# Kernel optimization log

Measured on AMD Instinct MI355X. Metric: run time of the kernel, lower is better.

Reference implementation:

```python
import jax, jax.numpy as jnp
import numpy as np

B, T, D, H = 4, 2048, 1024, 16
HD = D // H  # head dim = 64

def setup_inputs() -> dict:
    key = jax.random.key(0)
    ks = jax.random.split(key, 4)
    scale = 1.0 / np.sqrt(D)
    return {
        "hidden_states": jax.random.normal(ks[0], (B, T, D), dtype=jnp.float32),
        "attention_mask": jnp.zeros((B, 1, 1, T), dtype=jnp.float32),
        "Wq": jax.random.normal(ks[1], (D, D), dtype=jnp.float32) * scale,
        "bq": jnp.zeros((D,), dtype=jnp.float32),
        "Wk": jax.random.normal(ks[2], (D, D), dtype=jnp.float32) * scale,
        "bk": jnp.zeros((D,), dtype=jnp.float32),
        "Wv": jax.random.normal(ks[3], (D, D), dtype=jnp.float32) * scale,
        "bv": jnp.zeros((D,), dtype=jnp.float32),
    }

def _split_heads(x):
    # [B, T, D] -> [B, H, T, HD]
    b, t, _ = x.shape
    return x.reshape(b, t, H, HD).transpose(0, 2, 1, 3)

def reference(hidden_states, attention_mask, Wq, bq, Wk, bk, Wv, bv):
    q = _split_heads(hidden_states @ Wq.T + bq)
    k = _split_heads(hidden_states @ Wk.T + bk)
    v = _split_heads(hidden_states @ Wv.T + bv)
    # scores: [B, H, T, T]
    scores = jnp.einsum("bhqd,bhkd->bhqk", q, k) * (HD ** -0.5)
    t = hidden_states.shape[1]
    causal = jnp.triu(jnp.ones((t, t), dtype=bool), k=1)  # True above diagonal -> masked
    scores = jnp.where(causal[None, None], -jnp.inf, scores)
    scores = scores + attention_mask  # additive padding mask [B,1,1,T]
    probs = jax.nn.softmax(scores, axis=-1)
    out = jnp.einsum("bhqk,bhkd->bhqd", probs, v)
    # [B, H, T, HD] -> [B, T, D]
    return out.transpose(0, 2, 1, 3).reshape(hidden_states.shape[0], t, D)
```

## Files before the change

kernel.cpp:

```cpp
#include <hip/hip_runtime.h>
#include <hip/hip_bf16.h>
#include <stdint.h>

#define TT 2048
#define DD 1024
#define HH 16
#define HDIM 64
#define BB 4
#define MROWS 8192
#define LOG2E 1.44269504088896340736f

typedef __attribute__((ext_vector_type(8))) short short8;
typedef __attribute__((ext_vector_type(4))) float floatx4;

__device__ __forceinline__ ushort f2bf(float f){
  uint32_t u = __builtin_bit_cast(uint32_t, f);
  u = u + 0x7fffu + ((u >> 16) & 1u);
  return (ushort)(u >> 16);
}
__device__ __forceinline__ float bf2f(ushort s){
  uint32_t u = ((uint32_t)s) << 16;
  return __builtin_bit_cast(float, u);
}

__device__ __forceinline__ uint32_t cvtpk(float lo, float hi){
  uint32_t r;
  asm("v_cvt_pk_bf16_f32 %0, %1, %2" : "=v"(r) : "v"(lo), "v"(hi));
  return r;
}

__device__ __forceinline__ float exp2a(float x){
  float r;
  asm("v_exp_f32 %0, %1" : "=v"(r) : "v"(x));
  return r;
}

__device__ __forceinline__ void gld16(const void* g, void* l){
  __builtin_amdgcn_global_load_lds((const __attribute__((address_space(1))) uint32_t*)g,
                                   (__attribute__((address_space(3))) uint32_t*)l, 16, 0, 0);
}

__global__ void cvt_bf16(const float* __restrict__ src, ushort* __restrict__ dst, int n4){
  int i = blockIdx.x*blockDim.x + threadIdx.x;
  if (i < n4){
    float4 v = ((const float4*)src)[i];
    ushort4 o;
    o.x = f2bf(v.x); o.y = f2bf(v.y); o.z = f2bf(v.z); o.w = f2bf(v.w);
    ((ushort4*)dst)[i] = o;
  }
}

__global__ void cvt_w3(const float* __restrict__ wq, const float* __restrict__ wk,
                       const float* __restrict__ wv, ushort* __restrict__ dst){
  int m = blockIdx.y;
  const float* s = (m==0)? wq : (m==1? wk : wv);
  int i = blockIdx.x*blockDim.x + threadIdx.x;
  float4 v = ((const float4*)s)[i];
  ushort4 o;
  o.x = f2bf(v.x); o.y = f2bf(v.y); o.z = f2bf(v.z); o.w = f2bf(v.w);
  ((ushort4*)(dst + (size_t)m*DD*DD))[i] = o;
}

__global__ void w2_prep(const float* __restrict__ am, ushort* __restrict__ w2){
  int i = blockIdx.x*blockDim.x + threadIdx.x;
  if (i < BB*TT) w2[i] = f2bf(__expf(am[i]));
}

__global__ __launch_bounds__(256) void qkv_gemm(
    const ushort* __restrict__ A, const ushort* __restrict__ Wall,
    const float* __restrict__ bq, const float* __restrict__ bk, const float* __restrict__ bv,
    const ushort* __restrict__ w2,
    ushort* __restrict__ Qo, ushort* __restrict__ Ko, ushort* __restrict__ Vo)
{
  __shared__ __align__(16) ushort sA[128*64];
  __shared__ __align__(16) ushort sB[128*64];
  const int mat = blockIdx.z;
  const ushort* W = Wall + (size_t)mat*DD*DD;
  const float* bias = (mat==0)? bq : (mat==1? bk : bv);
  ushort* out = (mat==0)? Qo : (mat==1? Ko : Vo);
  const float oscale = (mat==0)? 0.125f*LOG2E : 1.0f;
  const bool matV = (mat == 2);
  const int m0 = blockIdx.x*128, n0 = blockIdx.y*128;
  const int tid = threadIdx.x, lane = tid & 63, wid = tid >> 6;
  const int wm = (wid>>1)*64, wn = (wid&1)*64;
  const int c = lane & 15, g = lane >> 4;
  const int srow = lane >> 3;
  const int scol = (lane & 7) * 8;

  floatx4 acc[4][4];
  #pragma unroll
  for (int i=0;i<4;i++)
    #pragma unroll
    for(int j=0;j<4;j++) acc[i][j] = (floatx4){0.f,0.f,0.f,0.f};

  for (int k0 = 0; k0 < DD; k0 += 64){
    #pragma unroll
    for (int j=0;j<4;j++){
      int chunk = wid*4 + j;
      int row = chunk*8 + srow;
      gld16(A + (size_t)(m0+row)*DD + k0 + scol, sA + chunk*512);
      gld16(W + (size_t)(n0+row)*DD + k0 + scol, sB + chunk*512);
    }
    __syncthreads();
    #pragma unroll
    for (int ch=0; ch<2; ++ch){
      short8 af[4], bfr[4];
      #pragma unroll
      for (int mf=0; mf<4; ++mf)
        af[mf] = *(const short8*)(sA + (wm + mf*16 + c)*64 + ch*32 + g*8);
      #pragma unroll
      for (int nf=0; nf<4; ++nf)
        bfr[nf] = *(const short8*)(sB + (wn + nf*16 + c)*64 + ch*32 + g*8);
      if (matV){
        #pragma unroll
        for (int mf=0; mf<4; ++mf)
          #pragma unroll
          for (int nf=0; nf<4; ++nf)
            acc[mf][nf] = __builtin_amdgcn_mfma_f32_16x16x32_bf16(af[mf], bfr[nf], acc[mf][nf], 0,0,0);
      } else {
        #pragma unroll
        for (int mf=0; mf<4; ++mf)
          #pragma unroll
          for (int nf=0; nf<4; ++nf)
            acc[mf][nf] = __builtin_amdgcn_mfma_f32_16x16x32_bf16(bfr[nf], af[mf], acc[mf][nf], 0,0,0);
      }
    }
    __syncthreads();
  }

  if (matV){
    #pragma unroll
    for (int nf=0; nf<4; ++nf){
      int col = n0 + wn + nf*16 + c;
      float bval = bias[col];
      int h = col >> 6, hd = col & 63;
      #pragma unroll
      for (int mf=0; mf<4; ++mf){
        int rowb = m0 + wm + mf*16 + g*4;
        int b = rowb >> 11, t = rowb & (TT-1);
        ushort4 wv = *(const ushort4*)(w2 + (size_t)b*TT + t);
        ushort4 st;
        st.x = f2bf((acc[mf][nf][0] + bval) * bf2f(wv.x));
        st.y = f2bf((acc[mf][nf][1] + bval) * bf2f(wv.y));
        st.z = f2bf((acc[mf][nf][2] + bval) * bf2f(wv.z));
        st.w = f2bf((acc[mf][nf][3] + bval) * bf2f(wv.w));
        *(ushort4*)(out + ((size_t)(b*HH + h)*HDIM + hd)*TT + t) = st;
      }
    }
  } else {
    #pragma unroll
    for (int nf=0; nf<4; ++nf){
      int feat = n0 + wn + nf*16 + g*4;
      float4 b4 = *(const float4*)(bias + feat);
      int h = feat >> 6, hd = feat & 63;
      #pragma unroll
      for (int mf=0; mf<4; ++mf){
        int trow = m0 + wm + mf*16 + c;
        int b = trow >> 11, t = trow & (TT-1);
        ushort4 st;
        st.x = f2bf((acc[mf][nf][0] + b4.x) * oscale);
        st.y = f2bf((acc[mf][nf][1] + b4.y) * oscale);
        st.z = f2bf((acc[mf][nf][2] + b4.z) * oscale);
        st.w = f2bf((acc[mf][nf][3] + b4.w) * oscale);
        *(ushort4*)(out + ((size_t)(b*HH + h)*TT + t)*HDIM + hd) = st;
      }
    }
  }
}

__global__ __launch_bounds__(256,3) void attn_fwd(
    const ushort* __restrict__ Q, const ushort* __restrict__ K, const ushort* __restrict__ VT,
    const ushort* __restrict__ W2, float* __restrict__ O)
{
  __shared__ __align__(16) ushort sKt[2][4096];
  __shared__ __align__(16) ushort sVt[2][4096];
  __shared__ __align__(16) uint32_t sP[4][256];

  const int bh = blockIdx.x, b = bh >> 4, h = bh & 15;
  const int pr = blockIdx.y;
  const int qt1 = pr, qt2 = 31 - pr;
  const int nt1 = qt1 + 1;
  const int ntot = qt1 + qt2 + 2;
  const int tid = threadIdx.x, lane = tid & 63, w = tid >> 6;
  const int c = lane & 15, g = lane >> 4;
  uint32_t* sPw = sP[w];

  const char* Kbh = (const char*)(K  + (size_t)bh*TT*HDIM);
  const char* Vbh = (const char*)(VT + (size_t)bh*HDIM*TT);
  const ushort* w2b = W2 + (size_t)b*TT;

  auto stage = [&](int f){
    int it = (f >= nt1) ? f - nt1 : f;
    int kv0 = it*64;
    int buf = f & 1;
    int rlo = w*8 + (lane>>3);
    int colb = (lane & 7)*16;
    #pragma unroll
    for (int j=0;j<2;++j){
      int row = j*32 + rlo;
      int sw = (row & 7) << 4;
      gld16(Kbh + (size_t)(kv0+row)*128 + (colb ^ sw), &sKt[buf][j*2048 + w*512]);
      gld16(Vbh + (size_t)row*(TT*2) + (size_t)kv0*2 + (colb ^ sw), &sVt[buf][j*2048 + w*512]);
    }
  };

  short8 qf[2];
  floatx4 oacc[4], lacc;
  float mreg;
  int qmy = qt1*64 + w*16 + c;

  auto loadq = [&](int qt_){
    qmy = qt_*64 + w*16 + c;
    #pragma unroll
    for (int ch=0; ch<2; ++ch)
      qf[ch] = *(const short8*)(Q + ((size_t)bh*TT + qmy)*HDIM + ch*32 + g*8);
  };
  auto reset_state = [&](){
    mreg = -1e30f;
    lacc = (floatx4){0.f,0.f,0.f,0.f};
    #pragma unroll
    for (int d=0; d<4; ++d) oacc[d] = (floatx4){0.f,0.f,0.f,0.f};
  };
  auto writeout = [&](){
    float rl = 1.f / lacc[0];
    #pragma unroll
    for (int d=0; d<4; ++d){
      float4 st;
      st.x = oacc[d][0]*rl; st.y = oacc[d][1]*rl;
      st.z = oacc[d][2]*rl; st.w = oacc[d][3]*rl;
      *(float4*)(O + ((size_t)b*TT + qmy)*DD + h*HDIM + d*16 + g*4) = st;
    }
  };

  loadq(qt1);
  reset_state();
  stage(0);

  int qt = qt1;
  for (int f=0; f<ntot; ++f){
    if (f == nt1){
      writeout();
      reset_state();
      loadq(qt2);
      qt = qt2;
    }
    const int it = (f >= nt1) ? f - nt1 : f;
    const int kv0 = it*64;

    short8 wfr[2];
    wfr[0] = *(const short8*)(w2b + kv0 + g*8);
    wfr[1] = *(const short8*)(w2b + kv0 + 32 + g*8);
    if (f+1 < ntot){
      stage(f+1);
      asm volatile("s_waitcnt vmcnt(4)" ::: "memory");
    } else {
      asm volatile("s_waitcnt vmcnt(0)" ::: "memory");
    }
    __builtin_amdgcn_s_barrier();
    __builtin_amdgcn_sched_barrier(0);

    const ushort* bK = sKt[f&1];
    const ushort* bV = sVt[f&1];
    const int rsw = (c & 7) << 3;

    short8 kf[2][4];
    #pragma unroll
    for (int ch=0; ch<2; ++ch)
      #pragma unroll
      for (int nt=0; nt<4; ++nt)
        kf[ch][nt] = *(const short8*)(bK + (nt*16 + c)*64 + ((ch*32 + g*8) ^ rsw));

    floatx4 sacc[4];
    #pragma unroll
    for (int i=0;i<4;i++) sacc[i] = (floatx4){0.f,0.f,0.f,0.f};
    __builtin_amdgcn_s_setprio(1);
    #pragma unroll
    for (int ch=0; ch<2; ++ch)
      #pragma unroll
      for (int nt=0; nt<4; ++nt)
        sacc[nt] = __builtin_amdgcn_mfma_f32_16x16x32_bf16(kf[ch][nt], qf[ch], sacc[nt], 0,0,0);
    __builtin_amdgcn_s_setprio(0);

    float p[4][4];
    float mx = -1e30f;
    if (it == qt){
      #pragma unroll
      for (int nt=0; nt<4; ++nt)
        #pragma unroll
        for (int r=0; r<4; ++r){
          int kv = kv0 + nt*16 + g*4 + r;
          float s = (kv > qmy) ? -1e30f : sacc[nt][r];
          p[nt][r] = s;
          mx = fmaxf(mx, s);
        }
    } else {
      #pragma unroll
      for (int nt=0; nt<4; ++nt)
        #pragma unroll
        for (int r=0; r<4; ++r){
          p[nt][r] = sacc[nt][r];
          mx = fmaxf(mx, sacc[nt][r]);
        }
    }
    mx = fmaxf(mx, __shfl_xor(mx, 16));
    mx = fmaxf(mx, __shfl_xor(mx, 32));
    if (!__all(mx <= mreg + 8.f)){
      float mn = fmaxf(mreg, mx);
      float sc = exp2a(mreg - mn);
      mreg = mn;
      lacc *= sc;
      #pragma unroll
      for (int d=0; d<4; ++d)
        #pragma unroll
        for (int r=0; r<4; ++r) oacc[d][r] *= sc;
    }
    #pragma unroll
    for (int nt=0; nt<4; ++nt)
      #pragma unroll
      for (int r=0; r<4; ++r)
        p[nt][r] = exp2a(p[nt][r] - mreg);

    short8 pbr[2];
    #pragma unroll
    for (int half=0; half<2; ++half){
      #pragma unroll
      for (int nt2=0; nt2<2; ++nt2){
        int nt = half*2 + nt2;
        int dl = c + 16*(nt2*2 + (g>>1));
        uint2 pk;
        pk.x = cvtpk(p[nt][0], p[nt][1]);
        pk.y = cvtpk(p[nt][2], p[nt][3]);
        *(uint2*)(sPw + dl*4 + (g&1)*2) = pk;
      }
      pbr[half] = *(const short8*)((const ushort*)sPw + lane*8);
    }

    short8 vf[2][4];
    #pragma unroll
    for (int ch=0; ch<2; ++ch)
      #pragma unroll
      for (int d=0; d<4; ++d)
        vf[ch][d] = *(const short8*)(bV + (d*16 + c)*64 + ((ch*32 + g*8) ^ rsw));
    __builtin_amdgcn_s_setprio(1);
    #pragma unroll
    for (int d=0; d<4; ++d)
      #pragma unroll
      for (int ch=0; ch<2; ++ch)
        oacc[d] = __builtin_amdgcn_mfma_f32_16x16x32_bf16(vf[ch][d], pbr[ch], oacc[d], 0,0,0);
    #pragma unroll
    for (int ch=0; ch<2; ++ch)
      lacc = __builtin_amdgcn_mfma_f32_16x16x32_bf16(wfr[ch], pbr[ch], lacc, 0,0,0);
    __builtin_amdgcn_s_setprio(0);

    __builtin_amdgcn_sched_barrier(0);
    __builtin_amdgcn_s_barrier();
  }
  writeout();
}

extern "C" void kernel_launch(void* const* d_in, const int* in_sizes, int n_in,
                              void* d_out, int out_size, void* d_ws, size_t ws_size,
                              hipStream_t stream){
  const float* hs    = (const float*)d_in[0];
  const float* amask = (const float*)d_in[1];
  const float* Wq    = (const float*)d_in[2];
  const float* bq    = (const float*)d_in[3];
  const float* Wk    = (const float*)d_in[4];
  const float* bk    = (const float*)d_in[5];
  const float* Wv    = (const float*)d_in[6];
  const float* bv    = (const float*)d_in[7];
  float* out = (float*)d_out;

  ushort* hsb = (ushort*)d_ws;
  ushort* wb  = hsb + (size_t)MROWS*DD;
  ushort* qb  = wb  + (size_t)3*DD*DD;
  ushort* kb  = qb  + (size_t)MROWS*DD;
  ushort* vtb = kb  + (size_t)MROWS*DD;
  ushort* w2b = vtb + (size_t)MROWS*DD;

  cvt_bf16<<<(MROWS*DD/4)/256, 256, 0, stream>>>(hs, hsb, MROWS*DD/4);
  cvt_w3<<<dim3((DD*DD/4)/256, 3), 256, 0, stream>>>(Wq, Wk, Wv, wb);
  w2_prep<<<(BB*TT)/256, 256, 0, stream>>>(amask, w2b);

  qkv_gemm<<<dim3(MROWS/128, DD/128, 3), 256, 0, stream>>>(hsb, wb, bq, bk, bv, w2b, qb, kb, vtb);
  attn_fwd<<<dim3(64, 16), 256, 0, stream>>>(qb, kb, vtb, w2b, out);
}
```

Before: 162.1 us.

## Double-buffer LDS tiles in QKV GEMM to overlap global loads with MFMA

Doubles the shared-memory tiles in the QKV projection GEMM and issues the next K-tile's global-to-LDS loads before computing on the current tile. Explicit vmcnt waits and raw barriers replace __syncthreads, so memory latency is meant to overlap with MFMA work. LDS use doubles to 64KB per block, which can lower occupancy. Only the projection GEMM changes; the attention kernel is untouched.

```diff
diff --git a/kernel.cpp b/kernel.cpp
--- a/kernel.cpp
+++ b/kernel.cpp
@@ -72,8 +72,8 @@
     const ushort* __restrict__ w2,
     ushort* __restrict__ Qo, ushort* __restrict__ Ko, ushort* __restrict__ Vo)
 {
-  __shared__ __align__(16) ushort sA[128*64];
-  __shared__ __align__(16) ushort sB[128*64];
+  __shared__ __align__(16) ushort sA[2][128*64];
+  __shared__ __align__(16) ushort sB[2][128*64];
   const int mat = blockIdx.z;
   const ushort* W = Wall + (size_t)mat*DD*DD;
   const float* bias = (mat==0)? bq : (mat==1? bk : bv);
@@ -93,24 +93,38 @@
     #pragma unroll
     for(int j=0;j<4;j++) acc[i][j] = (floatx4){0.f,0.f,0.f,0.f};
 
-  for (int k0 = 0; k0 < DD; k0 += 64){
+  auto stage = [&](int k0, int buf){
     #pragma unroll
     for (int j=0;j<4;j++){
       int chunk = wid*4 + j;
       int row = chunk*8 + srow;
-      gld16(A + (size_t)(m0+row)*DD + k0 + scol, sA + chunk*512);
-      gld16(W + (size_t)(n0+row)*DD + k0 + scol, sB + chunk*512);
-    }
-    __syncthreads();
+      gld16(A + (size_t)(m0+row)*DD + k0 + scol, sA[buf] + chunk*512);
+      gld16(W + (size_t)(n0+row)*DD + k0 + scol, sB[buf] + chunk*512);
+    }
+  };
+
+  stage(0, 0);
+  for (int kt = 0; kt < 16; ++kt){
+    if (kt+1 < 16){
+      stage((kt+1)*64, (kt+1)&1);
+      asm volatile("s_waitcnt vmcnt(8)" ::: "memory");
+    } else {
+      asm volatile("s_waitcnt vmcnt(0)" ::: "memory");
+    }
+    __builtin_amdgcn_s_barrier();
+    __builtin_amdgcn_sched_barrier(0);
+
+    const ushort* cA = sA[kt&1];
+    const ushort* cB = sB[kt&1];
     #pragma unroll
     for (int ch=0; ch<2; ++ch){
       short8 af[4], bfr[4];
       #pragma unroll
       for (int mf=0; mf<4; ++mf)
-        af[mf] = *(const short8*)(sA + (wm + mf*16 + c)*64 + ch*32 + g*8);
+        af[mf] = *(const short8*)(cA + (wm + mf*16 + c)*64 + ch*32 + g*8);
       #pragma unroll
       for (int nf=0; nf<4; ++nf)
-        bfr[nf] = *(const short8*)(sB + (wn + nf*16 + c)*64 + ch*32 + g*8);
+        bfr[nf] = *(const short8*)(cB + (wn + nf*16 + c)*64 + ch*32 + g*8);
       if (matV){
         #pragma unroll
         for (int mf=0; mf<4; ++mf)
@@ -125,7 +139,8 @@
             acc[mf][nf] = __builtin_amdgcn_mfma_f32_16x16x32_bf16(bfr[nf], af[mf], acc[mf][nf], 0,0,0);
       }
     }
-    __syncthreads();
+    __builtin_amdgcn_sched_barrier(0);
+    __builtin_amdgcn_s_barrier();
   }
 
   if (matV){
```

Measured after the change: 157.4 us. 2.9% less time.
